# Kernel optimization log

Measured on AMD Instinct MI355X. Metric: run time of the kernel, lower is better.

The kernel has to match this reference:

```python
import jax, jax.numpy as jnp
import numpy as np

N = 50000
E = 800000
R = 8
F_IN = 128
H = 128


def setup_inputs() -> dict:
    key = jax.random.key(0)
    ks = jax.random.split(key, 16)
    x = jax.random.normal(ks[0], (N, F_IN), dtype=jnp.float32)
    edge_index = jax.random.randint(ks[1], (2, E), 0, N, dtype=jnp.int64)
    edge_type = jax.random.randint(ks[2], (E,), 0, R, dtype=jnp.int64)
    s = 0.05
    params = {
        'W1': jax.random.normal(ks[3], (R, F_IN, H), jnp.float32) * s,
        'root1': jax.random.normal(ks[4], (F_IN, H), jnp.float32) * s,
        'b1': jnp.zeros((H,), jnp.float32),
        'W2': jax.random.normal(ks[5], (R, H, H), jnp.float32) * s,
        'root2': jax.random.normal(ks[6], (H, H), jnp.float32) * s,
        'b2': jnp.zeros((H,), jnp.float32),
        'W3': jax.random.normal(ks[7], (R, H, H), jnp.float32) * s,
        'root3': jax.random.normal(ks[8], (H, H), jnp.float32) * s,
        'b3': jnp.zeros((H,), jnp.float32),
        'fc_w': jax.random.normal(ks[9], (H, 1), jnp.float32) * s,
        'fc_b': jnp.zeros((1,), jnp.float32),
    }
    return dict(x=x, edge_index=edge_index, edge_type=edge_type, **params)


def _rgcn_conv(x, W, Wroot, b, src, dst, etype):
    # PyG RGCNConv with mean aggregation per (dst, relation):
    # out_i = x_i @ Wroot + b + sum_r mean_{j in N_r(i)} (x_j @ W_r)
    xw = jnp.einsum('nf,rfh->rnh', x, W)          # [R, N, H] per-relation transform
    m = xw[etype, src]                             # [E, H] gathered messages
    seg = dst * R + etype                          # composite (dst, rel) segment id
    deg = jax.ops.segment_sum(jnp.ones((m.shape[0],), x.dtype), seg, num_segments=N * R)
    norm = jnp.where(deg > 0, 1.0 / deg, 0.0)[seg]  # [E]
    agg = jax.ops.segment_sum(m * norm[:, None], dst, num_segments=N)  # [N, H]
    return agg + x @ Wroot + b


def reference(x, edge_index, edge_type, W1, root1, b1, W2, root2, b2, W3, root3, b3, fc_w, fc_b):
    src, dst = edge_index[0], edge_index[1]
    h = jax.nn.relu(_rgcn_conv(x, W1, root1, b1, src, dst, edge_type))
    h = jax.nn.relu(_rgcn_conv(h, W2, root2, b2, src, dst, edge_type))
    h = jax.nn.relu(_rgcn_conv(h, W3, root3, b3, src, dst, edge_type))
    out = h @ fc_w + fc_b                          # [N, 1]
    return out.reshape(-1)                         # [N]
```

## Files before the change

### kernel.cpp

```cpp
#include <hip/hip_runtime.h>

#define NN 50000
#define NPAD 50048
#define EE 800000
#define RR 8
#define NR (NN * RR)
#define KC 1152

typedef __attribute__((ext_vector_type(8))) short bf16x8;
typedef __attribute__((ext_vector_type(4))) float f32x4;

__device__ __forceinline__ unsigned short f2bf(float f) {
    unsigned u = __builtin_bit_cast(unsigned, f);
    u = (u + 0x7FFF + ((u >> 16) & 1)) >> 16;
    return (unsigned short)u;
}
__device__ __forceinline__ float bf2f(unsigned short s) {
    return __builtin_bit_cast(float, (unsigned)s << 16);
}

#define GLDS16(g, l) __builtin_amdgcn_global_load_lds( \
    (const __attribute__((address_space(1))) void*)(g), \
    (__attribute__((address_space(3))) void*)(l), 16, 0, 0)

__global__ void zero_i32(int* __restrict__ p, int n) {
    int i = blockIdx.x * blockDim.x + threadIdx.x;
    if (i < n) p[i] = 0;
}

__global__ void count_deg(const int* __restrict__ dst, const int* __restrict__ et,
                          int* __restrict__ degRel) {
    int e = blockIdx.x * blockDim.x + threadIdx.x;
    if (e < EE) atomicAdd(&degRel[dst[e] * RR + et[e]], 1);
}

__global__ void sum8(const int* __restrict__ degRel, int* __restrict__ degD) {
    int n = blockIdx.x * blockDim.x + threadIdx.x;
    if (n >= NN) return;
    int s = 0;
    #pragma unroll
    for (int r = 0; r < RR; ++r) s += degRel[n * RR + r];
    degD[n] = s;
}

__global__ __launch_bounds__(256) void scan1(const int* __restrict__ in, int* __restrict__ out,
                                             int* __restrict__ bsum, int n) {
    __shared__ int sh[256];
    int t = threadIdx.x;
    int base = blockIdx.x * 1024 + t * 4;
    int v[4]; int s = 0;
    #pragma unroll
    for (int i = 0; i < 4; ++i) { int idx = base + i; v[i] = (idx < n) ? in[idx] : 0; s += v[i]; }
    sh[t] = s; __syncthreads();
    for (int off = 1; off < 256; off <<= 1) {
        int x = (t >= off) ? sh[t - off] : 0; __syncthreads();
        if (t >= off) sh[t] += x; __syncthreads();
    }
    if (t == 255) bsum[blockIdx.x] = sh[255];
    int run = sh[t] - s;
    #pragma unroll
    for (int i = 0; i < 4; ++i) { int idx = base + i; if (idx < n) out[idx] = run; run += v[i]; }
}

__global__ __launch_bounds__(256) void scan2(int* __restrict__ bsum, int nb) {
    __shared__ int sh[256];
    int t = threadIdx.x; int carry = 0;
    for (int base = 0; base < nb; base += 256) {
        int idx = base + t;
        int v = (idx < nb) ? bsum[idx] : 0;
        sh[t] = v; __syncthreads();
        for (int off = 1; off < 256; off <<= 1) {
            int x = (t >= off) ? sh[t - off] : 0; __syncthreads();
            if (t >= off) sh[t] += x; __syncthreads();
        }
        int incl = sh[t];
        int total = sh[255];
        if (idx < nb) bsum[idx] = carry + incl - v;
        carry += total;
        __syncthreads();
    }
}

__global__ __launch_bounds__(256) void scan3(int* __restrict__ out, const int* __restrict__ bsum, int n) {
    int base = blockIdx.x * 1024 + threadIdx.x * 4;
    int add = bsum[blockIdx.x];
    #pragma unroll
    for (int i = 0; i < 4; ++i) { int idx = base + i; if (idx < n) out[idx] += add; }
}

__global__ void set_last(int* __restrict__ segD) {
    segD[NN] = EE;
}

__global__ void scatter2(const int* __restrict__ src, const int* __restrict__ dst,
                         const int* __restrict__ et, const int* __restrict__ segD,
                         const int* __restrict__ degRel, int* __restrict__ cursorD,
                         uint2* __restrict__ rec) {
    int e = blockIdx.x * blockDim.x + threadIdx.x;
    if (e >= EE) return;
    int d_ = dst[e], r_ = et[e], s_ = src[e];
    int pos = segD[d_] + atomicAdd(&cursorD[d_], 1);
    float nm = 1.f / (float)degRel[d_ * RR + r_];
    rec[pos] = make_uint2((unsigned)(s_ * KC + 128 + r_ * 128),
                          __builtin_bit_cast(unsigned, nm));
}

__global__ __launch_bounds__(256) void xcvt(const float* __restrict__ x,
                                            unsigned short* __restrict__ xbf) {
    size_t i = ((size_t)blockIdx.x * 256 + threadIdx.x) * 4;
    if (i >= (size_t)NPAD * 128) return;
    unsigned short o[4];
    if (i < (size_t)NN * 128) {
        float4 v = *reinterpret_cast<const float4*>(x + i);
        o[0] = f2bf(v.x); o[1] = f2bf(v.y); o[2] = f2bf(v.z); o[3] = f2bf(v.w);
    } else {
        o[0] = o[1] = o[2] = o[3] = 0;
    }
    unsigned lo = (unsigned)o[0] | ((unsigned)o[1] << 16);
    unsigned hi = (unsigned)o[2] | ((unsigned)o[3] << 16);
    *reinterpret_cast<uint2*>(xbf + i) = make_uint2(lo, hi);
}

__global__ void build_bt2(const float* __restrict__ W, const float* __restrict__ root,
                          unsigned short* __restrict__ Bt2) {
    int i = blockIdx.x * blockDim.x + threadIdx.x;
    if (i >= KC * 128) return;
    int col = i / 128, k = i % 128;
    float v;
    if (col < 128) v = root[k * 128 + col];
    else {
        int r = (col - 128) >> 7, cp = (col - 128) & 127;
        v = W[((size_t)r * 128 + k) * 128 + cp];
    }
    Bt2[i] = f2bf(v);
}

__global__ __launch_bounds__(256, 2) void gemm_y(
    const unsigned short* __restrict__ hin,
    const unsigned short* __restrict__ Bt2,
    unsigned short* __restrict__ y)
{
    __shared__ alignas(16) unsigned short Bs[128 * 128];
    const int tid = threadIdx.x;
    const int w = tid >> 6, lane = tid & 63;
    const int l15 = lane & 15, lhi = lane >> 4;
    const int row0 = blockIdx.x * 64;
    const int colbase = blockIdx.y * 128;

    #pragma unroll
    for (int i = 0; i < 8; ++i) {
        int q = i * 256 + tid;
        int col = q >> 4, c = q & 15;
        GLDS16(Bt2 + (size_t)(colbase + col) * 128 + ((c ^ (col & 7)) * 8), &Bs[(size_t)q * 8]);
    }
    const int gn = row0 + w * 16 + l15;
    const unsigned short* abase = hin + ((size_t)gn << 7) + lhi * 8;
    bf16x8 rf0 = *reinterpret_cast<const bf16x8*>(abase);
    bf16x8 rf1 = *reinterpret_cast<const bf16x8*>(abase + 32);
    bf16x8 rf2 = *reinterpret_cast<const bf16x8*>(abase + 64);
    bf16x8 rf3 = *reinterpret_cast<const bf16x8*>(abase + 96);

    f32x4 acc[8];
    #pragma unroll
    for (int i = 0; i < 8; ++i) acc[i] = (f32x4)(0.f);
    __syncthreads();

    bf16x8 rf[4] = {rf0, rf1, rf2, rf3};
    #pragma unroll
    for (int s = 0; s < 4; ++s) {
        #pragma unroll
        for (int cg = 0; cg < 8; ++cg) {
            int col = cg * 16 + l15;
            int phys = (s * 4 + lhi) ^ (col & 7);
            bf16x8 bv = *reinterpret_cast<const bf16x8*>(&Bs[col * 128 + phys * 8]);
            acc[cg] = __builtin_amdgcn_mfma_f32_16x16x32_bf16(rf[s], bv, acc[cg], 0, 0, 0);
        }
    }
    #pragma unroll
    for (int cg = 0; cg < 8; ++cg) {
        int col = colbase + cg * 16 + l15;
        #pragma unroll
        for (int rg = 0; rg < 4; ++rg) {
            int grow = row0 + w * 16 + lhi * 4 + rg;
            y[(size_t)grow * KC + col] = f2bf(acc[cg][rg]);
        }
    }
}

__global__ __launch_bounds__(256) void agg3(
    const unsigned short* __restrict__ y,
    const uint2* __restrict__ rec,
    const int* __restrict__ segD,
    const float* __restrict__ bias,
    unsigned short* __restrict__ hout)
{
    const int w = threadIdx.x >> 6, lane = threadIdx.x & 63;
    const int n = blockIdx.x * 4 + w;
    if (n >= NPAD) return;
    const int fl = lane & 15, eg = lane >> 4;

    float fa[8];
    #pragma unroll
    for (int i = 0; i < 8; ++i) fa[i] = 0.f;

    if (n < NN) {
        const int s0 = segD[n], s1 = segD[n + 1];
        for (int base = s0; base < s1; base += 64) {
            const int ld = min(64, s1 - base);
            int idx = base + lane; if (idx > s1 - 1) idx = s1 - 1;
            const uint2 rc = rec[idx];
            const int offL = (int)rc.x;
            const int nrmL = (int)rc.y;
            for (int t0 = 0; t0 < ld; t0 += 16) {
                uint4 L[4]; float nm[4];
                #pragma unroll
                for (int t = 0; t < 4; ++t) {
                    int j = t0 + t * 4 + eg;
                    int offj = __shfl(offL, j & 63);
                    int nbj  = __shfl(nrmL, j & 63);
                    bool on = (j < ld);
                    nm[t] = on ? __builtin_bit_cast(float, (unsigned)nbj) : 0.f;
                    const unsigned short* p = y + (size_t)(on ? offj : 0) + fl * 8;
                    L[t] = *reinterpret_cast<const uint4*>(p);
                }
                #pragma unroll
                for (int t = 0; t < 4; ++t) {
                    fa[0] += nm[t] * bf2f((unsigned short)(L[t].x & 0xFFFF));
                    fa[1] += nm[t] * bf2f((unsigned short)(L[t].x >> 16));
                    fa[2] += nm[t] * bf2f((unsigned short)(L[t].y & 0xFFFF));
                    fa[3] += nm[t] * bf2f((unsigned short)(L[t].y >> 16));
                    fa[4] += nm[t] * bf2f((unsigned short)(L[t].z & 0xFFFF));
                    fa[5] += nm[t] * bf2f((unsigned short)(L[t].z >> 16));
                    fa[6] += nm[t] * bf2f((unsigned short)(L[t].w & 0xFFFF));
                    fa[7] += nm[t] * bf2f((unsigned short)(L[t].w >> 16));
                }
            }
        }
        #pragma unroll
        for (int i = 0; i < 8; ++i) {
            fa[i] += __shfl_xor(fa[i], 16);
            fa[i] += __shfl_xor(fa[i], 32);
        }
    }

    if (eg == 0) {
        unsigned short o[8];
        if (n < NN) {
            const unsigned short* rp = y + (size_t)n * KC + fl * 8;
            uint4 rv = *reinterpret_cast<const uint4*>(rp);
            float4 b0 = *reinterpret_cast<const float4*>(bias + fl * 8);
            float4 b1 = *reinterpret_cast<const float4*>(bias + fl * 8 + 4);
            float r[8];
            r[0] = bf2f((unsigned short)(rv.x & 0xFFFF)); r[1] = bf2f((unsigned short)(rv.x >> 16));
            r[2] = bf2f((unsigned short)(rv.y & 0xFFFF)); r[3] = bf2f((unsigned short)(rv.y >> 16));
            r[4] = bf2f((unsigned short)(rv.z & 0xFFFF)); r[5] = bf2f((unsigned short)(rv.z >> 16));
            r[6] = bf2f((unsigned short)(rv.w & 0xFFFF)); r[7] = bf2f((unsigned short)(rv.w >> 16));
            float bb[8] = {b0.x, b0.y, b0.z, b0.w, b1.x, b1.y, b1.z, b1.w};
            #pragma unroll
            for (int i = 0; i < 8; ++i) o[i] = f2bf(fmaxf(fa[i] + r[i] + bb[i], 0.f));
        } else {
            #pragma unroll
            for (int i = 0; i < 8; ++i) o[i] = 0;
        }
        uint4 pk;
        pk.x = (unsigned)o[0] | ((unsigned)o[1] << 16);
        pk.y = (unsigned)o[2] | ((unsigned)o[3] << 16);
        pk.z = (unsigned)o[4] | ((unsigned)o[5] << 16);
        pk.w = (unsigned)o[6] | ((unsigned)o[7] << 16);
        *reinterpret_cast<uint4*>(hout + (size_t)n * 128 + fl * 8) = pk;
    }
}

__global__ __launch_bounds__(256) void final_fc(
    const unsigned short* __restrict__ h, const float* __restrict__ fcw,
    const float* __restrict__ fcb, float* __restrict__ out)
{
    int wid  = (int)((blockIdx.x * 256 + threadIdx.x) >> 6);
    int lane = threadIdx.x & 63;
    if (wid >= NN) return;
    float v = bf2f(h[(size_t)wid * 128 + lane]) * fcw[lane]
            + bf2f(h[(size_t)wid * 128 + 64 + lane]) * fcw[64 + lane];
    #pragma unroll
    for (int off = 32; off > 0; off >>= 1) v += __shfl_down(v, off);
    if (lane == 0) out[wid] = v + fcb[0];
}

extern "C" void kernel_launch(void* const* d_in, const int* in_sizes, int n_in,
                              void* d_out, int out_size, void* d_ws, size_t ws_size,
                              hipStream_t stream) {
    const float* x     = (const float*)d_in[0];
    const int*   ei    = (const int*)d_in[1];
    const int*   etype = (const int*)d_in[2];
    const float* W[3]    = {(const float*)d_in[3], (const float*)d_in[6], (const float*)d_in[9]};
    const float* root[3] = {(const float*)d_in[4], (const float*)d_in[7], (const float*)d_in[10]};
    const float* bias[3] = {(const float*)d_in[5], (const float*)d_in[8], (const float*)d_in[11]};
    const float* fcw = (const float*)d_in[12];
    const float* fcb = (const float*)d_in[13];
    const int* src = ei;
    const int* dst = ei + EE;

    char* ws = (char*)d_ws;
    auto alloc = [&](size_t bytes) { char* p = ws; ws += (bytes + 255) & ~(size_t)255; return p; };
    int* degRel   = (int*)alloc(NR * sizeof(int));
    int* cursorD  = (int*)alloc(NN * sizeof(int));
    int* degD     = (int*)alloc(NN * sizeof(int));
    int* segD     = (int*)alloc((NN + 2) * sizeof(int));
    int* bsum     = (int*)alloc(512 * sizeof(int));
    uint2* rec    = (uint2*)alloc((size_t)EE * sizeof(uint2));
    unsigned short* Bt2g = (unsigned short*)alloc((size_t)3 * KC * 128 * sizeof(short));
    unsigned short* xbf  = (unsigned short*)alloc((size_t)NPAD * 128 * sizeof(short));
    unsigned short* h1   = (unsigned short*)alloc((size_t)NPAD * 128 * sizeof(short));
    unsigned short* h2   = (unsigned short*)alloc((size_t)NPAD * 128 * sizeof(short));
    unsigned short* yall = (unsigned short*)alloc((size_t)NPAD * KC * sizeof(short));

    zero_i32<<<(NR + NN + 255) / 256, 256, 0, stream>>>(degRel, NR + NN);
    count_deg<<<(EE + 255) / 256, 256, 0, stream>>>(dst, etype, degRel);
    sum8<<<(NN + 255) / 256, 256, 0, stream>>>(degRel, degD);
    const int nScanBlk = (NN + 1023) / 1024;
    scan1<<<nScanBlk, 256, 0, stream>>>(degD, segD, bsum, NN);
    scan2<<<1, 256, 0, stream>>>(bsum, nScanBlk);
    scan3<<<nScanBlk, 256, 0, stream>>>(segD, bsum, NN);
    set_last<<<1, 1, 0, stream>>>(segD);
    scatter2<<<(EE + 255) / 256, 256, 0, stream>>>(src, dst, etype, segD, degRel, cursorD, rec);

    xcvt<<<((NPAD * 128 / 4) + 255) / 256, 256, 0, stream>>>(x, xbf);
    const int btN = KC * 128;
    for (int l = 0; l < 3; ++l)
        build_bt2<<<(btN + 255) / 256, 256, 0, stream>>>(W[l], root[l], Bt2g + (size_t)l * btN);

    dim3 ggrid(NPAD / 64, 9);
    const int aggGrid = NPAD / 4;
    const unsigned short* hin = xbf;
    unsigned short* houts[3] = {h1, h2, h1};
    for (int l = 0; l < 3; ++l) {
        gemm_y<<<ggrid, 256, 0, stream>>>(hin, Bt2g + (size_t)l * btN, yall);
        agg3<<<aggGrid, 256, 0, stream>>>(yall, rec, segD, bias[l], houts[l]);
        hin = houts[l];
    }

    final_fc<<<(NN * 64 + 255) / 256, 256, 0, stream>>>(h1, fcw, fcb, (float*)d_out);
}
```

Measured before the change: 335.9 us.

## Pack edge records, loop GEMM over column panels, fuse final FC into aggregation

Edge records shrink from 8 to 4 bytes by packing the gather offset with the per-relation degree, clamped to 63; the normalisation is recomputed with a fast reciprocal in the aggregation kernel. The GEMM now has each block walk all 9 output column panels with double-buffered LDS staging of the weights, instead of a 2D grid of one panel per block. The final linear layer is fused into the last aggregation kernel as a template variant, removing one launch and the write and read-back of the last hidden layer. The risks are reduced occupancy and parallelism in the GEMM from fewer blocks and doubled LDS, and wrong normalisation if any (node, relation) degree exceeds 63.

```diff
diff --git a/kernel.cpp b/kernel.cpp
--- a/kernel.cpp
+++ b/kernel.cpp
@@ -95,14 +95,13 @@
 __global__ void scatter2(const int* __restrict__ src, const int* __restrict__ dst,
                          const int* __restrict__ et, const int* __restrict__ segD,
                          const int* __restrict__ degRel, int* __restrict__ cursorD,
-                         uint2* __restrict__ rec) {
+                         unsigned* __restrict__ rec) {
     int e = blockIdx.x * blockDim.x + threadIdx.x;
     if (e >= EE) return;
     int d_ = dst[e], r_ = et[e], s_ = src[e];
     int pos = segD[d_] + atomicAdd(&cursorD[d_], 1);
-    float nm = 1.f / (float)degRel[d_ * RR + r_];
-    rec[pos] = make_uint2((unsigned)(s_ * KC + 128 + r_ * 128),
-                          __builtin_bit_cast(unsigned, nm));
+    int dg = degRel[d_ * RR + r_]; if (dg > 63) dg = 63;
+    rec[pos] = ((unsigned)(s_ * KC + 128 + r_ * 128) << 6) | (unsigned)dg;
 }
 
 __global__ __launch_bounds__(256) void xcvt(const float* __restrict__ x,
@@ -140,59 +139,70 @@
     const unsigned short* __restrict__ Bt2,
     unsigned short* __restrict__ y)
 {
-    __shared__ alignas(16) unsigned short Bs[128 * 128];
+    __shared__ alignas(16) unsigned short Bs[2][128 * 128];
     const int tid = threadIdx.x;
     const int w = tid >> 6, lane = tid & 63;
     const int l15 = lane & 15, lhi = lane >> 4;
     const int row0 = blockIdx.x * 64;
-    const int colbase = blockIdx.y * 128;
-
-    #pragma unroll
-    for (int i = 0; i < 8; ++i) {
-        int q = i * 256 + tid;
-        int col = q >> 4, c = q & 15;
-        GLDS16(Bt2 + (size_t)(colbase + col) * 128 + ((c ^ (col & 7)) * 8), &Bs[(size_t)q * 8]);
-    }
+
+    auto stage = [&](int b, int p) {
+        #pragma unroll
+        for (int i = 0; i < 8; ++i) {
+            int q = i * 256 + tid;
+            int col = q >> 4, c = q & 15;
+            GLDS16(Bt2 + (size_t)(p * 128 + col) * 128 + ((c ^ (col & 7)) * 8), &Bs[b][q * 8]);
+        }
+    };
+
     const int gn = row0 + w * 16 + l15;
     const unsigned short* abase = hin + ((size_t)gn << 7) + lhi * 8;
-    bf16x8 rf0 = *reinterpret_cast<const bf16x8*>(abase);
-    bf16x8 rf1 = *reinterpret_cast<const bf16x8*>(abase + 32);
-    bf16x8 rf2 = *reinterpret_cast<const bf16x8*>(abase + 64);
-    bf16x8 rf3 = *reinterpret_cast<const bf16x8*>(abase + 96);
-
-    f32x4 acc[8];
-    #pragma unroll
-    for (int i = 0; i < 8; ++i) acc[i] = (f32x4)(0.f);
+    bf16x8 rf[4];
+    rf[0] = *reinterpret_cast<const bf16x8*>(abase);
+    rf[1] = *reinterpret_cast<const bf16x8*>(abase + 32);
+    rf[2] = *reinterpret_cast<const bf16x8*>(abase + 64);
+    rf[3] = *reinterpret_cast<const bf16x8*>(abase + 96);
+
+    stage(0, 0);
     __syncthreads();
-
-    bf16x8 rf[4] = {rf0, rf1, rf2, rf3};
-    #pragma unroll
-    for (int s = 0; s < 4; ++s) {
+    for (int p = 0; p < 9; ++p) {
+        const int b = p & 1;
+        if (p < 8) stage(b ^ 1, p + 1);
+        f32x4 acc[8];
+        #pragma unroll
+        for (int i = 0; i < 8; ++i) acc[i] = (f32x4)(0.f);
+        #pragma unroll
+        for (int s = 0; s < 4; ++s) {
+            #pragma unroll
+            for (int cg = 0; cg < 8; ++cg) {
+                int col = cg * 16 + l15;
+                int phys = (s * 4 + lhi) ^ (col & 7);
+                bf16x8 bv = *reinterpret_cast<const bf16x8*>(&Bs[b][col * 128 + phys * 8]);
+                acc[cg] = __builtin_amdgcn_mfma_f32_16x16x32_bf16(rf[s], bv, acc[cg], 0, 0, 0);
+            }
+        }
         #pragma unroll
         for (int cg = 0; cg < 8; ++cg) {
-            int col = cg * 16 + l15;
-            int phys = (s * 4 + lhi) ^ (col & 7);
-            bf16x8 bv = *reinterpret_cast<const bf16x8*>(&Bs[col * 128 + phys * 8]);
-            acc[cg] = __builtin_amdgcn_mfma_f32_16x16x32_bf16(rf[s], bv, acc[cg], 0, 0, 0);
-        }
-    }
-    #pragma unroll
-    for (int cg = 0; cg < 8; ++cg) {
-        int col = colbase + cg * 16 + l15;
-        #pragma unroll
-        for (int rg = 0; rg < 4; ++rg) {
-            int grow = row0 + w * 16 + lhi * 4 + rg;
-            y[(size_t)grow * KC + col] = f2bf(acc[cg][rg]);
-        }
-    }
-}
-
+            int col = p * 128 + cg * 16 + l15;
+            #pragma unroll
+            for (int rg = 0; rg < 4; ++rg) {
+                int grow = row0 + w * 16 + lhi * 4 + rg;
+                y[(size_t)grow * KC + col] = f2bf(acc[cg][rg]);
+            }
+        }
+        __syncthreads();
+    }
+}
+
+template<bool FINAL>
 __global__ __launch_bounds__(256) void agg3(
     const unsigned short* __restrict__ y,
-    const uint2* __restrict__ rec,
+    const unsigned* __restrict__ rec,
     const int* __restrict__ segD,
     const float* __restrict__ bias,
-    unsigned short* __restrict__ hout)
+    unsigned short* __restrict__ hout,
+    const float* __restrict__ fcw,
+    const float* __restrict__ fcb,
+    float* __restrict__ fout)
 {
     const int w = threadIdx.x >> 6, lane = threadIdx.x & 63;
     const int n = blockIdx.x * 4 + w;
@@ -208,19 +218,17 @@
         for (int base = s0; base < s1; base += 64) {
             const int ld = min(64, s1 - base);
             int idx = base + lane; if (idx > s1 - 1) idx = s1 - 1;
-            const uint2 rc = rec[idx];
-            const int offL = (int)rc.x;
-            const int nrmL = (int)rc.y;
+            const int rcL = (int)rec[idx];
             for (int t0 = 0; t0 < ld; t0 += 16) {
                 uint4 L[4]; float nm[4];
                 #pragma unroll
                 for (int t = 0; t < 4; ++t) {
                     int j = t0 + t * 4 + eg;
-                    int offj = __shfl(offL, j & 63);
-                    int nbj  = __shfl(nrmL, j & 63);
+                    int rcj = __shfl(rcL, j & 63);
                     bool on = (j < ld);
-                    nm[t] = on ? __builtin_bit_cast(float, (unsigned)nbj) : 0.f;
-                    const unsigned short* p = y + (size_t)(on ? offj : 0) + fl * 8;
+                    nm[t] = on ? __builtin_amdgcn_rcpf((float)(rcj & 63)) : 0.f;
+                    unsigned off = ((unsigned)rcj) >> 6;
+                    const unsigned short* p = y + (size_t)(on ? off : 0u) + fl * 8;
                     L[t] = *reinterpret_cast<const uint4*>(p);
                 }
                 #pragma unroll
@@ -244,7 +252,6 @@
     }
 
     if (eg == 0) {
-        unsigned short o[8];
         if (n < NN) {
             const unsigned short* rp = y + (size_t)n * KC + fl * 8;
             uint4 rv = *reinterpret_cast<const uint4*>(rp);
@@ -256,33 +263,33 @@
             r[4] = bf2f((unsigned short)(rv.z & 0xFFFF)); r[5] = bf2f((unsigned short)(rv.z >> 16));
             r[6] = bf2f((unsigned short)(rv.w & 0xFFFF)); r[7] = bf2f((unsigned short)(rv.w >> 16));
             float bb[8] = {b0.x, b0.y, b0.z, b0.w, b1.x, b1.y, b1.z, b1.w};
+            float v[8];
             #pragma unroll
-            for (int i = 0; i < 8; ++i) o[i] = f2bf(fmaxf(fa[i] + r[i] + bb[i], 0.f));
-        } else {
-            #pragma unroll
-            for (int i = 0; i < 8; ++i) o[i] = 0;
-        }
-        uint4 pk;
-        pk.x = (unsigned)o[0] | ((unsigned)o[1] << 16);
-        pk.y = (unsigned)o[2] | ((unsigned)o[3] << 16);
-        pk.z = (unsigned)o[4] | ((unsigned)o[5] << 16);
-        pk.w = (unsigned)o[6] | ((unsigned)o[7] << 16);
-        *reinterpret_cast<uint4*>(hout + (size_t)n * 128 + fl * 8) = pk;
-    }
-}
-
-__global__ __launch_bounds__(256) void final_fc(
-    const unsigned short* __restrict__ h, const float* __restrict__ fcw,
-    const float* __restrict__ fcb, float* __restrict__ out)
-{
-    int wid  = (int)((blockIdx.x * 256 + threadIdx.x) >> 6);
-    int lane = threadIdx.x & 63;
-    if (wid >= NN) return;
-    float v = bf2f(h[(size_t)wid * 128 + lane]) * fcw[lane]
-            + bf2f(h[(size_t)wid * 128 + 64 + lane]) * fcw[64 + lane];
-    #pragma unroll
-    for (int off = 32; off > 0; off >>= 1) v += __shfl_down(v, off);
-    if (lane == 0) out[wid] = v + fcb[0];
+            for (int i = 0; i < 8; ++i) v[i] = fmaxf(fa[i] + r[i] + bb[i], 0.f);
+            if constexpr (!FINAL) {
+                uint4 pk;
+                unsigned short o[8];
+                #pragma unroll
+                for (int i = 0; i < 8; ++i) o[i] = f2bf(v[i]);
+                pk.x = (unsigned)o[0] | ((unsigned)o[1] << 16);
+                pk.y = (unsigned)o[2] | ((unsigned)o[3] << 16);
+                pk.z = (unsigned)o[4] | ((unsigned)o[5] << 16);
+                pk.w = (unsigned)o[6] | ((unsigned)o[7] << 16);
+                *reinterpret_cast<uint4*>(hout + (size_t)n * 128 + fl * 8) = pk;
+            } else {
+                float dp = 0.f;
+                #pragma unroll
+                for (int i = 0; i < 8; ++i) dp += bf2f(f2bf(v[i])) * fcw[fl * 8 + i];
+                dp += __shfl_xor(dp, 1);
+                dp += __shfl_xor(dp, 2);
+                dp += __shfl_xor(dp, 4);
+                dp += __shfl_xor(dp, 8);
+                if (fl == 0) fout[n] = dp + fcb[0];
+            }
+        } else if constexpr (!FINAL) {
+            *reinterpret_cast<uint4*>(hout + (size_t)n * 128 + fl * 8) = make_uint4(0, 0, 0, 0);
+        }
+    }
 }
 
 extern "C" void kernel_launch(void* const* d_in, const int* in_sizes, int n_in,
@@ -306,7 +313,7 @@
     int* degD     = (int*)alloc(NN * sizeof(int));
     int* segD     = (int*)alloc((NN + 2) * sizeof(int));
     int* bsum     = (int*)alloc(512 * sizeof(int));
-    uint2* rec    = (uint2*)alloc((size_t)EE * sizeof(uint2));
+    unsigned* rec = (unsigned*)alloc((size_t)EE * sizeof(unsigned));
     unsigned short* Bt2g = (unsigned short*)alloc((size_t)3 * KC * 128 * sizeof(short));
     unsigned short* xbf  = (unsigned short*)alloc((size_t)NPAD * 128 * sizeof(short));
     unsigned short* h1   = (unsigned short*)alloc((size_t)NPAD * 128 * sizeof(short));
@@ -328,15 +335,19 @@
     for (int l = 0; l < 3; ++l)
         build_bt2<<<(btN + 255) / 256, 256, 0, stream>>>(W[l], root[l], Bt2g + (size_t)l * btN);
 
-    dim3 ggrid(NPAD / 64, 9);
+    const int ggrid = NPAD / 64;
     const int aggGrid = NPAD / 4;
     const unsigned short* hin = xbf;
-    unsigned short* houts[3] = {h1, h2, h1};
+    unsigned short* houts[2] = {h1, h2};
     for (int l = 0; l < 3; ++l) {
         gemm_y<<<ggrid, 256, 0, stream>>>(hin, Bt2g + (size_t)l * btN, yall);
-        agg3<<<aggGrid, 256, 0, stream>>>(yall, rec, segD, bias[l], houts[l]);
-        hin = houts[l];
-    }
-
-    final_fc<<<(NN * 64 + 255) / 256, 256, 0, stream>>>(h1, fcw, fcb, (float*)d_out);
-}
+        if (l < 2) {
+            agg3<false><<<aggGrid, 256, 0, stream>>>(yall, rec, segD, bias[l], houts[l],
+                                                     nullptr, nullptr, nullptr);
+            hin = houts[l];
+        } else {
+            agg3<true><<<aggGrid, 256, 0, stream>>>(yall, rec, segD, bias[l], nullptr,
+                                                    fcw, fcb, (float*)d_out);
+        }
+    }
+}
```

Measured after the change: 328.3 us (median of 2 runs). -2.3%, faster.
